# Performance work log

Hardware: AMD Instinct MI355X
Metric: run time of the kernel (lower is better)

## Reference

```python
import jax, jax.numpy as jnp
from jax import lax
import numpy as np


def tridiagonal_solve(K, f):
    """Batched Thomas-algorithm solve of A(K) u = f.

    K: [..., m] diffusion coefficient at m grid points.
    f: broadcastable to [..., m-1] right-hand side.
    Returns u: [..., m-1].
    """
    n = K.shape[-1] - 1  # number of unknowns
    h2 = 1.0 / (n * n)
    f = jnp.broadcast_to(f, (*K.shape[:-1], n))

    denom0 = 2.0 * K[..., 0] + K[..., 1]
    c0 = -K[..., 1] / denom0  # [...]
    u0 = f[..., 0] / denom0

    # Forward elimination sweep, j = 1 .. n-2, as a scan over the grid axis.
    Kj = jnp.moveaxis(K[..., 1:n - 1], -1, 0)   # [n-2, ...] = K[..., j]
    Kj1 = jnp.moveaxis(K[..., 2:n], -1, 0)      # [n-2, ...] = K[..., j+1]
    fj = jnp.moveaxis(f[..., 1:n - 1], -1, 0)   # [n-2, ...]

    def fwd_step(carry, x):
        c_prev, u_prev = carry
        kj, kj1, fv = x
        denom = kj + kj1 + kj * c_prev
        c = -kj1 / denom
        u = (fv + kj * u_prev) / denom
        return (c, u), (c, u)

    _, (cs, us) = lax.scan(fwd_step, (c0, u0), (Kj, Kj1, fj))
    c_all = jnp.concatenate([c0[None], cs], axis=0)  # [n-1, ...] indices 0..n-2
    u_all = jnp.concatenate([u0[None], us], axis=0)  # [n-1, ...]

    Kn1 = K[..., n - 1]
    u_last = (f[..., n - 1] + Kn1 * u_all[-1]) / (Kn1 + Kn1 * c_all[-1])  # u[n-1]

    # Back substitution: u[j] -= c[j] * u[j+1], j = n-2 .. 0 (reverse scan).
    def bwd_step(u_next, x):
        cj, uj = x
        u_new = uj - cj * u_next
        return u_new, u_new

    _, u_head = lax.scan(bwd_step, u_last, (c_all, u_all), reverse=True)  # [n-1, ...]
    u_full = jnp.concatenate([u_head, u_last[None]], axis=0)  # [n, ...]
    return h2 * jnp.moveaxis(u_full, 0, -1)


def setup_inputs() -> dict:
    key = jax.random.key(0)
    k1, k2 = jax.random.split(key)
    B, M = 16384, 1024  # batch, grid points (n = M - 1 unknowns)
    alpha = jax.random.normal(k1, (B, M), dtype=jnp.float32)
    f_rhs = jax.random.normal(k2, (M - 1,), dtype=jnp.float32)
    return {"alpha": alpha, "f_rhs": f_rhs}


def reference(alpha, f_rhs):
    # DiffusionModel1d.forward: u = A(exp(alpha))^{-1} f_rhs
    return tridiagonal_solve(jnp.exp(alpha), f_rhs)
```

## Files before the change

### kernel.cpp

```cpp
#include <hip/hip_runtime.h>
#include <math.h>


constexpr int BT   = 16384;
constexpr int MPTS = 1024;
constexpr int NU   = 1023;
constexpr int CS   = 16;
constexpr int WPB  = 4;

__device__ __forceinline__ float frcp(float x) {
    float r = __builtin_amdgcn_rcpf(x);
    r = fmaf(r, fmaf(-x, r, 1.0f), r);
    return r;
}
__device__ __forceinline__ double drcp(double x) {
    double r = __builtin_amdgcn_rcp(x);
    r = fma(r, fma(-x, r, 1.0), r);
    return r;
}

__global__ __launch_bounds__(WPB * 64, 4)
void pt_kernel(const float* __restrict__ alpha,
               const float* __restrict__ f_rhs,
               float* __restrict__ out) {
    const int t    = threadIdx.x;
    const int lane = t & 63;
    const int w    = t >> 6;
    const int row  = blockIdx.x * WPB + w;
    const int s    = lane * CS;

    __shared__ float ostage[WPB][NU + (NU >> 5) + 2];
    __shared__ float f_lds[1056];

    for (int i = t; i < NU; i += WPB * 64) f_lds[i + (i >> 5)] = f_rhs[i];
    if (t == 0) f_lds[1023 + (1023 >> 5)] = 0.0f;

    const float* arow = alpha + (size_t)row * MPTS;
    float kf[CS + 1];
    #pragma unroll
    for (int q = 0; q < 4; ++q) {
        const float4 v = *reinterpret_cast<const float4*>(arow + s + 4 * q);
        kf[4 * q + 0] = expf(v.x);
        kf[4 * q + 1] = expf(v.y);
        kf[4 * q + 2] = expf(v.z);
        kf[4 * q + 3] = expf(v.w);
    }
    {
        float kx = (lane < 63) ? arow[s + CS] : 0.0f;
        kf[CS] = expf(kx);
    }
    if (lane == 63) kf[15] = 0.0f;

    __syncthreads();

    float cA[CS], uA[CS], vA[CS];
    {
        float cp = (lane == 0) ? 1.0f : 0.0f;
        float up = 0.0f, vp = 1.0f;
        #pragma unroll
        for (int i = 0; i < CS; ++i) {
            const int j = s + i;
            const float kc = kf[i];
            const float kn = kf[i + 1];
            const float b  = kc + kn;
            const float f  = f_lds[j + (j >> 5)];
            const float den = fmaf(kc, cp, b);
            const float r   = frcp(den);
            float ci = -kn * r;
            const float ui = fmaf(kc, up, f) * r;
            const float vi = (kc * vp) * r;
            if (i == CS - 1) ci = (lane == 63) ? 0.0f : ci;
            cA[i] = ci; uA[i] = ui; vA[i] = vi;
            cp = ci; up = ui; vp = vi;
        }
    }

    float De_f, Ae_f, Be_f, Ds_f, As_f, Bs_f;
    {
        float Dn = uA[CS - 1], An = vA[CS - 1], Bn = -cA[CS - 1];
        De_f = Dn; Ae_f = An; Be_f = Bn;
        uA[CS - 1] = Dn; vA[CS - 1] = An; cA[CS - 1] = Bn;
        #pragma unroll
        for (int i = CS - 2; i >= 0; --i) {
            const float ci = cA[i];
            Dn = fmaf(-ci, Dn, uA[i]);
            An = fmaf(-ci, An, vA[i]);
            Bn = -ci * Bn;
            uA[i] = Dn; vA[i] = An; cA[i] = Bn;
        }
        Ds_f = uA[0]; As_f = vA[0]; Bs_f = cA[0];
    }

    const double Ds = (double)Ds_f, As = (double)As_f, Bs = (double)Bs_f;
    const double De = (double)De_f, Ae = (double)Ae_f, Be = (double)Be_f;
    double m00 = Bs;
    double m01 = fma(Bs, De, -(Ds * Be));
    double m02 = Ds;
    double m11 = fma(Bs, Ae, -(As * Be));
    double m12 = As;
    double m21 = -Be;

    #pragma unroll
    for (int dlt = 1; dlt < 64; dlt <<= 1) {
        const bool val = (lane + dlt) < 64;
        double b00 = __shfl_down(m00, dlt); b00 = val ? b00 : 1.0;
        double b01 = __shfl_down(m01, dlt); b01 = val ? b01 : 0.0;
        double b02 = __shfl_down(m02, dlt); b02 = val ? b02 : 0.0;
        double b11 = __shfl_down(m11, dlt); b11 = val ? b11 : 1.0;
        double b12 = __shfl_down(m12, dlt); b12 = val ? b12 : 0.0;
        double b21 = __shfl_down(m21, dlt); b21 = val ? b21 : 0.0;
        const double n00 = m00 * b00;
        const double n01 = fma(m00, b01, fma(m01, b11, m02 * b21));
        const double n02 = fma(m00, b02, fma(m01, b12, m02));
        const double n11 = fma(m11, b11, m12 * b21);
        const double n12 = fma(m11, b12, m12);
        const double n21 = fma(m21, b11, b21);
        const double n22 = fma(m21, b12, 1.0);
        const double rn = drcp(n22);
        m00 = n00 * rn; m01 = n01 * rn; m02 = n02 * rn;
        m11 = n11 * rn; m12 = n12 * rn; m21 = n21 * rn;
    }
    const double alf = m02;
    const double bet = m12;
    double alfn = __shfl_down(alf, 1); alfn = (lane == 63) ? 0.0 : alfn;
    double betn = __shfl_down(bet, 1); betn = (lane == 63) ? 0.0 : betn;

    const double tt = drcp(fma(-Be, betn, 1.0));
    const double dl = fma(Be, alfn, De) * tt;
    const double gm = Ae * tt;

    double X = dl, G = gm;
    #pragma unroll
    for (int dlt = 1; dlt < 64; dlt <<= 1) {
        double bx = __shfl_up(X, dlt);
        double bg = __shfl_up(G, dlt);
        const bool val = lane >= dlt;
        bx = val ? bx : 0.0;
        bg = val ? bg : 1.0;
        X = fma(G, bx, X);
        G = G * bg;
    }
    double xp = __shfl_up(X, 1);
    const double uLd = (lane == 0) ? 0.0 : xp;
    const double Y   = fma(bet, uLd, alf);
    double yn = __shfl_down(Y, 1);
    const double uRd = (lane == 63) ? 0.0 : yn;

    const float uL = (float)uLd;
    const float uR = (float)uRd;
    const float h2 = (float)(1.0 / (1023.0 * 1023.0));
    float* ost = ostage[w];
    #pragma unroll
    for (int i = 0; i < CS; ++i) {
        const int j = s + i;
        const float uu = fmaf(vA[i], uL, fmaf(cA[i], uR, uA[i]));
        if (j < NU) ost[j + (j >> 5)] = h2 * uu;
    }
    __syncthreads();

    float* orow = out + (size_t)row * NU;
    #pragma unroll
    for (int it = 0; it < 16; ++it) {
        const int c = it * 64 + lane;
        if (c < NU) orow[c] = ost[c + (c >> 5)];
    }
}

extern "C" void kernel_launch(void* const* d_in, const int* in_sizes, int n_in,
                              void* d_out, int out_size, void* d_ws, size_t ws_size,
                              hipStream_t stream) {
    const float* alpha = (const float*)d_in[0];
    const float* f_rhs = (const float*)d_in[1];
    float* out = (float*)d_out;

    dim3 grid(BT / WPB), block(WPB * 64);
    pt_kernel<<<grid, block, 0, stream>>>(alpha, f_rhs, out);
}
```

Baseline: 38.68 us.

## Recompute local chunk solve instead of storing three coefficient arrays

Replaces the stored forward sweep plus backward pass with two interleaved forward and reverse sweeps that produce only the chunk boundary coefficients, so the cA/uA/vA register arrays are no longer held across the shuffle scans. After the boundary values are known, a second local Thomas solve with the boundary terms folded into the right-hand side produces the outputs. The h2 scaling is moved into the f load. This lowers register pressure, which may allow higher occupancy, at the cost of roughly one extra sweep of reciprocals per chunk.

```diff
diff --git a/kernel.cpp b/kernel.cpp
--- a/kernel.cpp
+++ b/kernel.cpp
@@ -18,6 +18,7 @@
     r = fma(r, fma(-x, r, 1.0), r);
     return r;
 }
+__device__ __forceinline__ int sw(int j) { return j + (j >> 5); }
 
 __global__ __launch_bounds__(WPB * 64, 4)
 void pt_kernel(const float* __restrict__ alpha,
@@ -29,11 +30,12 @@
     const int row  = blockIdx.x * WPB + w;
     const int s    = lane * CS;
 
-    __shared__ float ostage[WPB][NU + (NU >> 5) + 2];
     __shared__ float f_lds[1056];
+    __shared__ float ostage[WPB][1056];
 
-    for (int i = t; i < NU; i += WPB * 64) f_lds[i + (i >> 5)] = f_rhs[i];
-    if (t == 0) f_lds[1023 + (1023 >> 5)] = 0.0f;
+    const float h2 = (float)(1.0 / (1023.0 * 1023.0));
+    for (int i = t; i < NU; i += WPB * 64) f_lds[sw(i)] = h2 * f_rhs[i];
+    if (t == 0) f_lds[sw(1023)] = 0.0f;
 
     const float* arow = alpha + (size_t)row * MPTS;
     float kf[CS + 1];
@@ -53,43 +55,42 @@
 
     __syncthreads();
 
-    float cA[CS], uA[CS], vA[CS];
-    {
-        float cp = (lane == 0) ? 1.0f : 0.0f;
-        float up = 0.0f, vp = 1.0f;
-        #pragma unroll
-        for (int i = 0; i < CS; ++i) {
-            const int j = s + i;
-            const float kc = kf[i];
-            const float kn = kf[i + 1];
+    float cF = (lane == 0) ? 1.0f : 0.0f, uF = 0.0f, vF = 1.0f;
+    float uRv = 0.0f, vRv = 1.0f, wRv = 0.0f;
+    #pragma unroll
+    for (int i = 0; i < CS; ++i) {
+        {
+            const float kc = kf[i], kn = kf[i + 1];
             const float b  = kc + kn;
-            const float f  = f_lds[j + (j >> 5)];
-            const float den = fmaf(kc, cp, b);
+            const float f  = f_lds[sw(s + i)];
+            const float den = fmaf(kc, cF, b);
             const float r   = frcp(den);
             float ci = -kn * r;
-            const float ui = fmaf(kc, up, f) * r;
-            const float vi = (kc * vp) * r;
+            const float ui = fmaf(kc, uF, f) * r;
+            const float vi = (kc * vF) * r;
             if (i == CS - 1) ci = (lane == 63) ? 0.0f : ci;
-            cA[i] = ci; uA[i] = ui; vA[i] = vi;
-            cp = ci; up = ui; vp = vi;
+            cF = ci; uF = ui; vF = vi;
+        }
+        {
+            const int ir = CS - 1 - i;
+            float kc = kf[ir];
+            const float kn = kf[ir + 1];
+            float b = kc + kn;
+            if (ir == 0) {
+                b  = (lane == 0) ? (b + kc) : b;
+                kc = (lane == 0) ? 0.0f : kc;
+            }
+            const float f  = f_lds[sw(s + ir)];
+            const float den = fmaf(-kn, wRv, b);
+            const float r   = frcp(den);
+            const float ui = fmaf(kn, uRv, f) * r;
+            const float vi = (kn * vRv) * r;
+            const float wi = kc * r;
+            uRv = ui; vRv = vi; wRv = wi;
         }
     }
-
-    float De_f, Ae_f, Be_f, Ds_f, As_f, Bs_f;
-    {
-        float Dn = uA[CS - 1], An = vA[CS - 1], Bn = -cA[CS - 1];
-        De_f = Dn; Ae_f = An; Be_f = Bn;
-        uA[CS - 1] = Dn; vA[CS - 1] = An; cA[CS - 1] = Bn;
-        #pragma unroll
-        for (int i = CS - 2; i >= 0; --i) {
-            const float ci = cA[i];
-            Dn = fmaf(-ci, Dn, uA[i]);
-            An = fmaf(-ci, An, vA[i]);
-            Bn = -ci * Bn;
-            uA[i] = Dn; vA[i] = An; cA[i] = Bn;
-        }
-        Ds_f = uA[0]; As_f = vA[0]; Bs_f = cA[0];
-    }
+    const float De_f = uF,  Ae_f = vF,  Be_f = -cF;
+    const float Ds_f = uRv, Bs_f = vRv, As_f = wRv;
 
     const double Ds = (double)Ds_f, As = (double)As_f, Bs = (double)Bs_f;
     const double De = (double)De_f, Ae = (double)Ae_f, Be = (double)Be_f;
@@ -148,13 +149,33 @@
 
     const float uL = (float)uLd;
     const float uR = (float)uRd;
-    const float h2 = (float)(1.0 / (1023.0 * 1023.0));
+    float c3[CS], u3[CS];
+    {
+        float cp = (lane == 0) ? 1.0f : 0.0f, up = 0.0f;
+        #pragma unroll
+        for (int i = 0; i < CS; ++i) {
+            const float kc = kf[i], kn = kf[i + 1];
+            const float b  = kc + kn;
+            float f = f_lds[sw(s + i)];
+            if (i == 0)      f = fmaf(kf[0],  uL, f);
+            if (i == CS - 1) f = fmaf(kf[CS], uR, f);
+            const float den = fmaf(kc, cp, b);
+            const float r   = frcp(den);
+            const float ci = -kn * r;
+            const float ui = fmaf(kc, up, f) * r;
+            c3[i] = ci; u3[i] = ui;
+            cp = ci; up = ui;
+        }
+    }
     float* ost = ostage[w];
-    #pragma unroll
-    for (int i = 0; i < CS; ++i) {
-        const int j = s + i;
-        const float uu = fmaf(vA[i], uL, fmaf(cA[i], uR, uA[i]));
-        if (j < NU) ost[j + (j >> 5)] = h2 * uu;
+    {
+        float un = u3[CS - 1];
+        ost[sw(s + CS - 1)] = un;
+        #pragma unroll
+        for (int i = CS - 2; i >= 0; --i) {
+            un = fmaf(-c3[i], un, u3[i]);
+            ost[sw(s + i)] = un;
+        }
     }
     __syncthreads();
 
@@ -162,7 +183,7 @@
     #pragma unroll
     for (int it = 0; it < 16; ++it) {
         const int c = it * 64 + lane;
-        if (c < NU) orow[c] = ost[c + (c >> 5)];
+        if (c < NU) orow[c] = ost[sw(c)];
     }
 }
 
```

Result: slower. 39.73 us (+2.7%).
